# Optimization experiments

Hardware: AMD Instinct MI355X
Metric: run time of the kernel (lower is better)

Reference implementation:

```python
import jax, jax.numpy as jnp
import numpy as np

# static config
B, H, W, C = 32, 56, 56, 128
WH, WW = 7, 7
SH, SW = 3, 3
NH = 4            # num heads
HD = C // NH      # head dim = 32
N = WH * WW       # 49 tokens per window
NWIN = (H // WH) * (W // WW)  # 64 windows
MLP_H = int(C * 4.0)
EPS = 1e-6
SCALE = HD ** -0.5


def _rel_pos_index():
    ch, cw = np.arange(WH), np.arange(WW)
    co = np.stack(np.meshgrid(ch, cw, indexing='ij')).reshape(2, -1)
    rc = (co[:, :, None] - co[:, None, :]).transpose(1, 2, 0)
    rc[:, :, 0] += WH - 1
    rc[:, :, 1] += WW - 1
    rc[:, :, 0] *= 2 * WW - 1
    return rc.sum(-1)  # [N, N] int


def _attn_mask():
    img = np.zeros((1, H, W, 1), np.float32)
    cnt = 0
    for hs in (slice(0, -WH), slice(-WH, -SH), slice(-SH, None)):
        for ws in (slice(0, -WW), slice(-WW, -SW), slice(-SW, None)):
            img[:, hs, ws, :] = cnt
            cnt += 1
    mw = img.reshape(1, H // WH, WH, W // WW, WW, 1)
    mw = mw.transpose(0, 1, 3, 2, 4, 5).reshape(-1, N)  # [nW, N]
    am = mw[:, None, :] - mw[:, :, None]
    return np.where(am != 0, -100.0, 0.0).astype(np.float32)  # [nW, N, N]

REL_IDX = jnp.asarray(_rel_pos_index())
ATTN_MASK = jnp.asarray(_attn_mask())


def _ln(x, g, b):
    mu = jnp.mean(x, -1, keepdims=True)
    var = jnp.mean(jnp.square(x - mu), -1, keepdims=True)
    return (x - mu) * jax.lax.rsqrt(var + EPS) * g + b


def _part(x):  # [B,H,W,C] -> [B*nW, N, C]
    x = x.reshape(B, H // WH, WH, W // WW, WW, C)
    return x.transpose(0, 1, 3, 2, 4, 5).reshape(-1, N, C)


def _rev(w):  # [B*nW, N, C] -> [B,H,W,C]
    x = w.reshape(B, H // WH, W // WW, WH, WW, C)
    return x.transpose(0, 1, 3, 2, 4, 5).reshape(B, H, W, C)


def setup_inputs() -> dict:
    key = jax.random.key(0)
    ks = jax.random.split(key, 16)
    s = lambda k, sh, sc=0.02: jax.random.normal(k, sh, jnp.float32) * sc
    return {
        'x': jax.random.normal(ks[0], (B, H * W, C), jnp.float32),
        'qkv_w': s(ks[1], (C, 3 * C)),
        'qkv_b': jnp.zeros((3 * C,), jnp.float32),
        'proj_w': s(ks[2], (C, C)),
        'proj_b': jnp.zeros((C,), jnp.float32),
        'proj_ln_g': jnp.ones((C,), jnp.float32),
        'proj_ln_b': jnp.zeros((C,), jnp.float32),
        'rpb_table': s(ks[3], ((2 * WH - 1) * (2 * WW - 1), NH)),
        'norm1_g': jnp.ones((C,), jnp.float32),
        'norm1_b': jnp.zeros((C,), jnp.float32),
        'norm2_g': jnp.ones((C,), jnp.float32),
        'norm2_b': jnp.zeros((C,), jnp.float32),
        'mlp_w1': s(ks[4], (C, MLP_H)),
        'mlp_b1': jnp.zeros((MLP_H,), jnp.float32),
        'mlp_w2': s(ks[5], (MLP_H, C)),
        'mlp_b2': jnp.zeros((C,), jnp.float32),
    }


def reference(x, qkv_w, qkv_b, proj_w, proj_b, proj_ln_g, proj_ln_b, rpb_table,
              norm1_g, norm1_b, norm2_g, norm2_b, mlp_w1, mlp_b1, mlp_w2, mlp_b2):
    shortcut = x
    h = _ln(x, norm1_g, norm1_b).reshape(B, H, W, C)
    h = jnp.roll(h, shift=(-SH, -SW), axis=(1, 2))        # cyclic shift
    w = _part(h)                                          # [B*nW, N, C]

    qkv = w @ qkv_w + qkv_b                               # [B*nW, N, 3C]
    qkv = qkv.reshape(-1, N, 3, NH, HD).transpose(2, 0, 3, 1, 4)
    q, k, v = qkv[0] * SCALE, qkv[1], qkv[2]              # [B*nW, NH, N, HD]
    attn = jnp.einsum('bhnd,bhmd->bhnm', q, k)            # [B*nW, NH, N, N]

    bias = rpb_table[REL_IDX.reshape(-1)].reshape(N, N, NH).transpose(2, 0, 1)
    attn = attn + bias[None]

    # masked path (shifted windows): NOTE source applies softmax TWICE — faithful
    attn = attn.reshape(-1, NWIN, NH, N, N) + ATTN_MASK[None, :, None]
    attn = jax.nn.softmax(attn, axis=-1)
    attn = attn.reshape(-1, NH, N, N)
    attn = jax.nn.softmax(attn, axis=-1)

    o = jnp.einsum('bhnm,bhmd->bhnd', attn, v)
    o = o.transpose(0, 2, 1, 3).reshape(-1, N, C)
    # projection: Dense -> LayerNorm -> GELU (as in source WindowAttention)
    o = jax.nn.gelu(_ln(o @ proj_w + proj_b, proj_ln_g, proj_ln_b), approximate=False)

    h = _rev(o)
    h = jnp.roll(h, shift=(SH, SW), axis=(1, 2)).reshape(B, H * W, C)
    x = shortcut + h

    m = _ln(x, norm2_g, norm2_b)
    m = jax.nn.gelu(m @ mlp_w1 + mlp_b1, approximate=False) @ mlp_w2 + mlp_b2
    return x + m
```

## Files before the change

### kernel.cpp

```cpp
#include <hip/hip_runtime.h>
#include <cstdint>
#include <cstddef>

typedef __attribute__((ext_vector_type(8))) short bf16x8;
typedef __attribute__((ext_vector_type(4))) float f32x4;
typedef unsigned char uchar;

namespace {
constexpr float kScale = 0.17677669529663689f;
constexpr float kEps = 1e-6f;
constexpr float kInvC = 1.0f / 128.0f;

__device__ __forceinline__ float gelu_fast(float v) {
  float t1 = fmaf(0.044715f * v, v, 1.0f);
  float x = v * t1 * -1.5957691216057308f;
  float e = __expf(x);
  return v * __builtin_amdgcn_rcpf(1.0f + e);
}
__device__ __forceinline__ float gelu_sig(float v) {
  float e = __expf(-1.702f * v);
  return v * __builtin_amdgcn_rcpf(1.0f + e);
}
__device__ __forceinline__ ushort f2bf(float f) {
  uint32_t u = __builtin_bit_cast(uint32_t, f);
  u += 0x7FFFu + ((u >> 16) & 1u);
  return (ushort)(u >> 16);
}
__device__ __forceinline__ float bf2f(ushort u) {
  return __builtin_bit_cast(float, (uint32_t)u << 16);
}
__device__ __forceinline__ void gl16(const void* g, void* l) {
  __builtin_amdgcn_global_load_lds(
      (const __attribute__((address_space(1))) void*)g,
      (__attribute__((address_space(3))) void*)l, 16, 0, 0);
}
__device__ __forceinline__ int map_row(int t) {
  int win = t / 49, nn = t - win * 49;
  int bb = win >> 6, wi = win & 63;
  int whi = wi >> 3, wwi = wi & 7;
  int r7 = nn / 7, c7 = nn - r7 * 7;
  int hs = whi * 7 + r7 + 3; if (hs >= 56) hs -= 56;
  int wsd = wwi * 7 + c7 + 3; if (wsd >= 56) wsd -= 56;
  return bb * 3136 + hs * 56 + wsd;
}
}

__global__ __launch_bounds__(256) void k_prep(
    const float* __restrict__ qkv_w, const float* __restrict__ w1,
    const float* __restrict__ w2, const float* __restrict__ pw,
    ushort* __restrict__ qkvT, ushort* __restrict__ w1T,
    uchar* __restrict__ w2T8, ushort* __restrict__ projT) {
  int i = blockIdx.x * 256 + threadIdx.x;
  if (i < 49152) {
    int n = i >> 7, k = i & 127;
    qkvT[i] = f2bf(qkv_w[k * 384 + n]);
  } else if (i < 114688) {
    int j = i - 49152;
    int n = j >> 7, k = j & 127;
    w1T[j] = f2bf(w1[k * 512 + n]);
  } else if (i < 147456) {
    int j = i - 114688;
    int n = j >> 8, k2 = (j & 255) << 1;
    int u = __builtin_amdgcn_cvt_pk_fp8_f32(w2[(size_t)k2 * 128 + n],
                                            w2[(size_t)(k2 + 1) * 128 + n], 0,
                                            false);
    w2T8[n * 512 + k2] = (uchar)u;
    w2T8[n * 512 + k2 + 1] = (uchar)(u >> 8);
  } else if (i < 163840) {
    int j = i - 147456;
    int n = j >> 7, k = j & 127;
    projT[j] = f2bf(pw[k * 128 + n]);
  }
}

__global__ __launch_bounds__(256) void k_prep2(
    const float* __restrict__ rpb, float* __restrict__ TB) {
  int e = blockIdx.x * 256 + threadIdx.x;
  int i = e & 63, j = (e >> 6) & 63, h = (e >> 12) & 3, type = e >> 14;
  float v = 0.f;
  if (i < 49 && j < 49) {
    int ri = i / 7, ci = i - ri * 7, rj = j / 7, cj = j - rj * 7;
    int ridx = (ri - rj + 6) * 13 + (ci - cj + 6);
    float bias = rpb[ridx * 4 + h];
    int th = type >> 1, tw = type & 1;
    int labi = (th ? ((ri < 4) ? 1 : 2) : 0) * 3 + (tw ? ((ci < 4) ? 1 : 2) : 0);
    int labj = (th ? ((rj < 4) ? 1 : 2) : 0) * 3 + (tw ? ((cj < 4) ? 1 : 2) : 0);
    v = bias + ((labi != labj) ? -100.f : 0.f);
  }
  TB[e] = v;
}

__global__ __launch_bounds__(256) void k_ln1_part(
    const float* __restrict__ x, const float* __restrict__ g,
    const float* __restrict__ b, ushort* __restrict__ wp) {
  int lane = threadIdx.x & 63, wv = threadIdx.x >> 6;
  int half = lane >> 5, l32 = lane & 31;
  int tok = blockIdx.x * 8 + wv * 2 + half;
  size_t src = (size_t)map_row(tok) * 128;
  float4 v = *(const float4*)(x + src + l32 * 4);
  float s = v.x + v.y + v.z + v.w;
  float sq = v.x * v.x + v.y * v.y + v.z * v.z + v.w * v.w;
#pragma unroll
  for (int off = 1; off < 32; off <<= 1) {
    s += __shfl_xor(s, off);
    sq += __shfl_xor(sq, off);
  }
  float mu = s * kInvC;
  float var = sq * kInvC - mu * mu;
  float rs = rsqrtf(var + kEps);
  float4 gg = *(const float4*)(g + l32 * 4);
  float4 bv = *(const float4*)(b + l32 * 4);
  float o0 = (v.x - mu) * rs * gg.x + bv.x;
  float o1 = (v.y - mu) * rs * gg.y + bv.y;
  float o2 = (v.z - mu) * rs * gg.z + bv.z;
  float o3 = (v.w - mu) * rs * gg.w + bv.w;
  uint2 p;
  p.x = (uint)f2bf(o0) | ((uint)f2bf(o1) << 16);
  p.y = (uint)f2bf(o2) | ((uint)f2bf(o3) << 16);
  ((uint2*)wp)[(size_t)tok * 32 + l32] = p;
}

template <int K, int LDC, int EPI>
__global__ __launch_bounds__(256) void k_gemm2(
    const ushort* __restrict__ A, const ushort* __restrict__ BT,
    const float* __restrict__ bias, ushort* __restrict__ C) {
  __shared__ ushort sbuf[12288];
  int tid = threadIdx.x;
  int nBase = blockIdx.x << 7;
  int mBase = blockIdx.y << 6;
  int lane = tid & 63, wid = tid >> 6;
  int li = lane & 15, g = lane >> 4;
  int wr = (wid >> 1) << 5, wc = (wid & 1) << 6;
  int swz = (li & 7) << 3;
  f32x4 acc[2][4] = {};
  for (int ks = 0; ks < K; ks += 64) {
#pragma unroll
    for (int l = 0; l < 2; ++l) {
      int c = l * 256 + tid;
      int row = c >> 3;
      int k8 = ((c & 7) ^ (row & 7)) << 3;
      gl16(A + (size_t)(mBase + row) * K + ks + k8,
           sbuf + (l * 256 + wid * 64) * 8);
    }
#pragma unroll
    for (int l = 0; l < 4; ++l) {
      int c = l * 256 + tid;
      int row = c >> 3;
      int k8 = ((c & 7) ^ (row & 7)) << 3;
      gl16(BT + (size_t)(nBase + row) * K + ks + k8,
           sbuf + 4096 + (l * 256 + wid * 64) * 8);
    }
    __syncthreads();
#pragma unroll
    for (int ksub = 0; ksub < 64; ksub += 32) {
      int kloc = ksub + g * 8;
      bf16x8 af[2], bfr[4];
#pragma unroll
      for (int m = 0; m < 2; ++m)
        af[m] = *(const bf16x8*)(sbuf + (wr + m * 16 + li) * 64 + (kloc ^ swz));
#pragma unroll
      for (int n = 0; n < 4; ++n)
        bfr[n] = *(const bf16x8*)(sbuf + 4096 + (wc + n * 16 + li) * 64 +
                                  (kloc ^ swz));
#pragma unroll
      for (int m = 0; m < 2; ++m)
#pragma unroll
        for (int n = 0; n < 4; ++n)
          acc[m][n] = __builtin_amdgcn_mfma_f32_16x16x32_bf16(
              af[m], bfr[n], acc[m][n], 0, 0, 0);
    }
    __syncthreads();
  }
#pragma unroll
  for (int n = 0; n < 4; ++n) {
    float bv = bias[nBase + wc + n * 16 + li];
    int col = wc + n * 16 + li;
#pragma unroll
    for (int m = 0; m < 2; ++m) {
      int rb = wr + m * 16 + (g << 2);
#pragma unroll
      for (int r = 0; r < 4; ++r) {
        float v = acc[m][n][r] + bv;
        if (EPI == 1) v = gelu_fast(v);
        sbuf[(rb + r) * 136 + col] = f2bf(v);
      }
    }
  }
  __syncthreads();
#pragma unroll
  for (int it = 0; it < 4; ++it) {
    int ch = tid + it * 256;
    int row = ch >> 4, c8 = (ch & 15) << 3;
    *(bf16x8*)(C + (size_t)(mBase + row) * LDC + nBase + c8) =
        *(const bf16x8*)(sbuf + row * 136 + c8);
  }
}

__global__ __launch_bounds__(256) void k_mlp1(
    const ushort* __restrict__ A, const ushort* __restrict__ BT,
    const float* __restrict__ bias, uchar* __restrict__ C8) {
  __shared__ ushort sbuf[12288];
  int tid = threadIdx.x;
  int nBase = blockIdx.x << 7;
  int mBase = blockIdx.y << 6;
  int lane = tid & 63, wid = tid >> 6;
  int li = lane & 15, g = lane >> 4;
  int wr = (wid >> 1) << 5, wc = (wid & 1) << 6;
  int swz = (li & 7) << 3;
  f32x4 acc[2][4] = {};
  for (int ks = 0; ks < 128; ks += 64) {
#pragma unroll
    for (int l = 0; l < 2; ++l) {
      int c = l * 256 + tid;
      int row = c >> 3;
      int k8 = ((c & 7) ^ (row & 7)) << 3;
      gl16(A + (size_t)(mBase + row) * 128 + ks + k8,
           sbuf + (l * 256 + wid * 64) * 8);
    }
#pragma unroll
    for (int l = 0; l < 4; ++l) {
      int c = l * 256 + tid;
      int row = c >> 3;
      int k8 = ((c & 7) ^ (row & 7)) << 3;
      gl16(BT + (size_t)(nBase + row) * 128 + ks + k8,
           sbuf + 4096 + (l * 256 + wid * 64) * 8);
    }
    __syncthreads();
#pragma unroll
    for (int ksub = 0; ksub < 64; ksub += 32) {
      int kloc = ksub + g * 8;
      bf16x8 af[2], bfr[4];
#pragma unroll
      for (int m = 0; m < 2; ++m)
        af[m] = *(const bf16x8*)(sbuf + (wr + m * 16 + li) * 64 + (kloc ^ swz));
#pragma unroll
      for (int n = 0; n < 4; ++n)
        bfr[n] = *(const bf16x8*)(sbuf + 4096 + (wc + n * 16 + li) * 64 +
                                  (kloc ^ swz));
#pragma unroll
      for (int m = 0; m < 2; ++m)
#pragma unroll
        for (int n = 0; n < 4; ++n)
          acc[m][n] = __builtin_amdgcn_mfma_f32_16x16x32_bf16(
              af[m], bfr[n], acc[m][n], 0, 0, 0);
    }
    __syncthreads();
  }
  uchar* Cs8 = (uchar*)sbuf;
#pragma unroll
  for (int n = 0; n < 4; ++n) {
    float bv = bias[nBase + wc + n * 16 + li];
    int col = wc + n * 16 + li;
#pragma unroll
    for (int m = 0; m < 2; ++m) {
      int rb = wr + m * 16 + (g << 2);
      float v0 = gelu_sig(acc[m][n][0] + bv);
      float v1 = gelu_sig(acc[m][n][1] + bv);
      float v2 = gelu_sig(acc[m][n][2] + bv);
      float v3 = gelu_sig(acc[m][n][3] + bv);
      int u01 = __builtin_amdgcn_cvt_pk_fp8_f32(v0, v1, 0, false);
      int u23 = __builtin_amdgcn_cvt_pk_fp8_f32(v2, v3, 0, false);
      Cs8[(rb + 0) * 144 + col] = (uchar)u01;
      Cs8[(rb + 1) * 144 + col] = (uchar)(u01 >> 8);
      Cs8[(rb + 2) * 144 + col] = (uchar)u23;
      Cs8[(rb + 3) * 144 + col] = (uchar)(u23 >> 8);
    }
  }
  __syncthreads();
#pragma unroll
  for (int it = 0; it < 2; ++it) {
    int ch = tid + it * 256;
    int row = ch >> 3, c16 = (ch & 7) << 4;
    *(bf16x8*)(C8 + (size_t)(mBase + row) * 512 + nBase + c16) =
        *(const bf16x8*)(Cs8 + row * 144 + c16);
  }
}

__global__ __launch_bounds__(256) void k_mlp2(
    const uchar* __restrict__ A8, const uchar* __restrict__ BT8,
    const float* __restrict__ bias, const ushort* __restrict__ resw,
    float* __restrict__ out) {
  __shared__ uchar sbuf[32768];
  __shared__ int mapr[64];
  int tid = threadIdx.x;
  int mBase = blockIdx.x << 6;
  if (tid < 64) mapr[tid] = map_row(mBase + tid);
  int lane = tid & 63, wid = tid >> 6;
  int li = lane & 15, g = lane >> 4;
  int wr = (wid >> 1) << 5, wc = (wid & 1) << 6;
  f32x4 acc[2][4] = {};
  for (int kb = 0; kb < 512; kb += 128) {
#pragma unroll
    for (int l = 0; l < 2; ++l) {
      int c = l * 256 + tid;
      int row = c >> 3;
      int ch = (c & 7) ^ (row & 7);
      gl16(A8 + (size_t)(mBase + row) * 512 + kb + (ch << 4),
           sbuf + (l * 256 + wid * 64) * 16);
    }
#pragma unroll
    for (int l = 0; l < 4; ++l) {
      int c = l * 256 + tid;
      int row = c >> 3;
      int ch = (c & 7) ^ (row & 7);
      gl16(BT8 + (size_t)row * 512 + kb + (ch << 4),
           sbuf + 8192 + (l * 256 + wid * 64) * 16);
    }
    __syncthreads();
#pragma unroll
    for (int ks = 0; ks < 4; ++ks) {
      int off = ks * 32 + g * 8;
      long long af[2], bfr[4];
#pragma unroll
      for (int m = 0; m < 2; ++m) {
        int r = wr + m * 16 + li;
        af[m] = *(const long long*)(sbuf + r * 128 + (off ^ ((r & 7) << 4)));
      }
#pragma unroll
      for (int n = 0; n < 4; ++n) {
        int rb = wc + n * 16 + li;
        bfr[n] = *(const long long*)(sbuf + 8192 + rb * 128 +
                                     (off ^ ((rb & 7) << 4)));
      }
#pragma unroll
      for (int m = 0; m < 2; ++m)
#pragma unroll
        for (int n = 0; n < 4; ++n)
          acc[m][n] = __builtin_amdgcn_mfma_f32_16x16x32_fp8_fp8(
              af[m], bfr[n], acc[m][n], 0, 0, 0);
    }
    __syncthreads();
  }
  float (*outs)[128] = (float(*)[128])sbuf;
#pragma unroll
  for (int n = 0; n < 4; ++n) {
    int cg = wc + n * 16 + li;
    float bv = bias[cg];
#pragma unroll
    for (int m = 0; m < 2; ++m) {
      int rb = wr + m * 16 + (g << 2);
#pragma unroll
      for (int r = 0; r < 4; ++r) {
        float rv = bf2f(resw[(size_t)(mBase + rb + r) * 128 + cg]);
        outs[rb + r][cg] = rv + acc[m][n][r] + bv;
      }
    }
  }
  __syncthreads();
#pragma unroll
  for (int it = 0; it < 8; ++it) {
    int ch = tid + it * 256;
    int row = ch >> 5, c4 = (ch & 31) << 2;
    *(float4*)(out + (size_t)mapr[row] * 128 + c4) =
        *(const float4*)&outs[row][c4];
  }
}

__global__ __launch_bounds__(256) void k_pgemm(
    const ushort* __restrict__ A, const ushort* __restrict__ BT,
    const float* __restrict__ pb, const float* __restrict__ lg,
    const float* __restrict__ lb, const float* __restrict__ x,
    const float* __restrict__ g2, const float* __restrict__ b2n,
    ushort* __restrict__ resw, ushort* __restrict__ wp) {
  __shared__ ushort sbuf[16384];
  __shared__ float red[4][64][2];
  __shared__ int mapr[64];
  int tid = threadIdx.x;
  int mBase = blockIdx.x << 6;
  if (tid < 64) mapr[tid] = map_row(mBase + tid);
  int lane = tid & 63, wid = tid >> 6;
  int li = lane & 15, g = lane >> 4;
  int wr = (wid >> 1) << 5, wc = (wid & 1) << 6;
  int swz = (li & 7) << 3;
  f32x4 acc[2][4] = {};
  for (int ks = 0; ks < 128; ks += 64) {
#pragma unroll
    for (int l = 0; l < 2; ++l) {
      int c = l * 256 + tid;
      int row = c >> 3;
      int k8 = ((c & 7) ^ (row & 7)) << 3;
      gl16(A + (size_t)(mBase + row) * 128 + ks + k8,
           sbuf + (l * 256 + wid * 64) * 8);
    }
#pragma unroll
    for (int l = 0; l < 4; ++l) {
      int c = l * 256 + tid;
      int row = c >> 3;
      int k8 = ((c & 7) ^ (row & 7)) << 3;
      gl16(BT + (size_t)row * 128 + ks + k8,
           sbuf + 4096 + (l * 256 + wid * 64) * 8);
    }
    __syncthreads();
#pragma unroll
    for (int ksub = 0; ksub < 64; ksub += 32) {
      int kloc = ksub + g * 8;
      bf16x8 af[2], bfr[4];
#pragma unroll
      for (int m = 0; m < 2; ++m)
        af[m] = *(const bf16x8*)(sbuf + (wr + m * 16 + li) * 64 + (kloc ^ swz));
#pragma unroll
      for (int n = 0; n < 4; ++n)
        bfr[n] = *(const bf16x8*)(sbuf + 4096 + (wc + n * 16 + li) * 64 +
                                  (kloc ^ swz));
#pragma unroll
      for (int m = 0; m < 2; ++m)
#pragma unroll
        for (int n = 0; n < 4; ++n)
          acc[m][n] = __builtin_amdgcn_mfma_f32_16x16x32_bf16(
              af[m], bfr[n], acc[m][n], 0, 0, 0);
    }
    __syncthreads();
  }
  float pbv[4], lgv[4], lbv[4], g2v[4], b2v[4];
#pragma unroll
  for (int n = 0; n < 4; ++n) {
    int cg = wc + n * 16 + li;
    pbv[n] = pb[cg]; lgv[n] = lg[cg]; lbv[n] = lb[cg];
    g2v[n] = g2[cg]; b2v[n] = b2n[cg];
  }
  float ps[2][4], psq[2][4];
#pragma unroll
  for (int m = 0; m < 2; ++m)
#pragma unroll
    for (int r = 0; r < 4; ++r) {
      float s = 0.f, q = 0.f;
#pragma unroll
      for (int n = 0; n < 4; ++n) {
        float v = acc[m][n][r] + pbv[n];
        s += v; q += v * v;
      }
#pragma unroll
      for (int off = 1; off < 16; off <<= 1) {
        s += __shfl_xor(s, off);
        q += __shfl_xor(q, off);
      }
      ps[m][r] = s; psq[m][r] = q;
    }
  if (li == 0) {
#pragma unroll
    for (int m = 0; m < 2; ++m)
#pragma unroll
      for (int r = 0; r < 4; ++r) {
        int rl = wr + m * 16 + (g << 2) + r;
        red[wid][rl][0] = ps[m][r];
        red[wid][rl][1] = psq[m][r];
      }
  }
  __syncthreads();
  float mu1[2][4], rs1[2][4];
#pragma unroll
  for (int m = 0; m < 2; ++m)
#pragma unroll
    for (int r = 0; r < 4; ++r) {
      int rl = wr + m * 16 + (g << 2) + r;
      float s = ps[m][r] + red[wid ^ 1][rl][0];
      float q = psq[m][r] + red[wid ^ 1][rl][1];
      mu1[m][r] = s * kInvC;
      rs1[m][r] = rsqrtf(q * kInvC - mu1[m][r] * mu1[m][r] + kEps);
    }
  __syncthreads();
#pragma unroll
  for (int m = 0; m < 2; ++m)
#pragma unroll
    for (int r = 0; r < 4; ++r) {
      int rowl = wr + m * 16 + (g << 2) + r;
      size_t xb = (size_t)mapr[rowl] * 128 + wc + li;
#pragma unroll
      for (int n = 0; n < 4; ++n) {
        float y = (acc[m][n][r] + pbv[n] - mu1[m][r]) * rs1[m][r] * lgv[n] +
                  lbv[n];
        acc[m][n][r] = gelu_fast(y) + x[xb + n * 16];
      }
    }
#pragma unroll
  for (int m = 0; m < 2; ++m)
#pragma unroll
    for (int r = 0; r < 4; ++r) {
      float s = 0.f, q = 0.f;
#pragma unroll
      for (int n = 0; n < 4; ++n) {
        float v = acc[m][n][r];
        s += v; q += v * v;
      }
#pragma unroll
      for (int off = 1; off < 16; off <<= 1) {
        s += __shfl_xor(s, off);
        q += __shfl_xor(q, off);
      }
      ps[m][r] = s; psq[m][r] = q;
    }
  if (li == 0) {
#pragma unroll
    for (int m = 0; m < 2; ++m)
#pragma unroll
      for (int r = 0; r < 4; ++r) {
        int rl = wr + m * 16 + (g << 2) + r;
        red[wid][rl][0] = ps[m][r];
        red[wid][rl][1] = psq[m][r];
      }
  }
  __syncthreads();
  ushort (*Cr)[128] = (ushort(*)[128])sbuf;
  ushort (*Cw)[128] = (ushort(*)[128])(sbuf + 8192);
#pragma unroll
  for (int m = 0; m < 2; ++m)
#pragma unroll
    for (int r = 0; r < 4; ++r) {
      int rl = wr + m * 16 + (g << 2) + r;
      float s = ps[m][r] + red[wid ^ 1][rl][0];
      float q = psq[m][r] + red[wid ^ 1][rl][1];
      float mu = s * kInvC;
      float rs = rsqrtf(q * kInvC - mu * mu + kEps);
#pragma unroll
      for (int n = 0; n < 4; ++n) {
        int col = wc + n * 16 + li;
        float rv = acc[m][n][r];
        Cr[rl][col] = f2bf(rv);
        Cw[rl][col] = f2bf((rv - mu) * rs * g2v[n] + b2v[n]);
      }
    }
  __syncthreads();
#pragma unroll
  for (int it = 0; it < 4; ++it) {
    int ch = tid + it * 256;
    int row = ch >> 4, c8 = (ch & 15) << 3;
    *(bf16x8*)(resw + (size_t)(mBase + row) * 128 + c8) =
        *(const bf16x8*)&Cr[row][c8];
    *(bf16x8*)(wp + (size_t)(mBase + row) * 128 + c8) =
        *(const bf16x8*)&Cw[row][c8];
  }
}

__global__ __launch_bounds__(256) void k_attn(
    const ushort* __restrict__ qkv, const float* __restrict__ TB,
    ushort* __restrict__ ob) {
  __shared__ ushort Pl[4][64][68];
  __shared__ ushort Vt[4][32][68];
  int tid = threadIdx.x;
  int lane = tid & 63, h = tid >> 6;
  int li = lane & 15, g = lane >> 4;
  int win = blockIdx.x;
  int wi = win & 63;
  int type = (((wi >> 3) == 7) ? 2 : 0) | (((wi & 7) == 7) ? 1 : 0);

  const ushort* qbase = qkv + (size_t)win * 49 * 384 + h * 32 + g * 8;
  bf16x8 kf[4], qf[4];
#pragma unroll
  for (int m = 0; m < 4; ++m) {
    kf[m] = *(const bf16x8*)(qbase + (size_t)(m * 16 + li) * 384 + 128);
    qf[m] = *(const bf16x8*)(qbase + (size_t)(m * 16 + li) * 384);
  }
  f32x4 zero = {0.f, 0.f, 0.f, 0.f};
  f32x4 st[4][4];
#pragma unroll
  for (int m = 0; m < 4; ++m)
#pragma unroll
    for (int n = 0; n < 4; ++n)
      st[m][n] = __builtin_amdgcn_mfma_f32_16x16x32_bf16(kf[m], qf[n], zero, 0, 0, 0);

  if (lane < 49) {
#pragma unroll
    for (int dc = 0; dc < 4; ++dc) {
      bf16x8 vv = *(const bf16x8*)(qkv + ((size_t)win * 49 + lane) * 384 + 256 +
                                   h * 32 + dc * 8);
#pragma unroll
      for (int t = 0; t < 8; ++t) Vt[h][dc * 8 + t][lane] = (ushort)vv[t];
    }
  } else {
#pragma unroll
    for (int d = 0; d < 32; ++d) Vt[h][d][lane] = 0;
  }

  const float* tb = TB + ((size_t)(type * 4 + h) << 12);
#pragma unroll
  for (int n = 0; n < 4; ++n) {
    int icol = n * 16 + li;
    float sv[3][4];
#pragma unroll
    for (int m = 0; m < 3; ++m)
#pragma unroll
      for (int r = 0; r < 4; ++r)
        sv[m][r] = st[m][n][r] * kScale + tb[(m * 16 + g * 4 + r) * 64 + icol];
    float sv3 = (g == 0) ? (st[3][n][0] * kScale + tb[48 * 64 + icol]) : -1e30f;
    float e[3][4], e3 = __expf(sv3);
    float sum = e3;
#pragma unroll
    for (int m = 0; m < 3; ++m)
#pragma unroll
      for (int r = 0; r < 4; ++r) { e[m][r] = __expf(sv[m][r]); sum += e[m][r]; }
    sum += __shfl_xor(sum, 16);
    sum += __shfl_xor(sum, 32);
    float inv = 1.f / sum;
    float e2[3][4];
    float e23 = (g == 0) ? __expf(e3 * inv) : 0.f;
    float sum2 = e23;
#pragma unroll
    for (int m = 0; m < 3; ++m)
#pragma unroll
      for (int r = 0; r < 4; ++r) { e2[m][r] = __expf(e[m][r] * inv); sum2 += e2[m][r]; }
    sum2 += __shfl_xor(sum2, 16);
    sum2 += __shfl_xor(sum2, 32);
    float inv2 = 1.f / sum2;
#pragma unroll
    for (int m = 0; m < 3; ++m) {
      uint u0 = (uint)f2bf(e2[m][0] * inv2) | ((uint)f2bf(e2[m][1] * inv2) << 16);
      uint u1 = (uint)f2bf(e2[m][2] * inv2) | ((uint)f2bf(e2[m][3] * inv2) << 16);
      *(uint*)&Pl[h][icol][m * 16 + g * 4]     = u0;
      *(uint*)&Pl[h][icol][m * 16 + g * 4 + 2] = u1;
    }
    uint u3 = (g == 0) ? (uint)f2bf(e23 * inv2) : 0u;
    *(uint*)&Pl[h][icol][48 + g * 4]     = u3;
    *(uint*)&Pl[h][icol][48 + g * 4 + 2] = 0u;
  }
  __syncthreads();

  f32x4 oacc[4][2] = {};
#pragma unroll
  for (int ks = 0; ks < 2; ++ks) {
    int kloc = ks * 32 + g * 8;
    bf16x8 bf0 = *(const bf16x8*)&Vt[h][li][kloc];
    bf16x8 bf1 = *(const bf16x8*)&Vt[h][16 + li][kloc];
#pragma unroll
    for (int mi = 0; mi < 4; ++mi) {
      bf16x8 af = *(const bf16x8*)&Pl[h][mi * 16 + li][kloc];
      oacc[mi][0] = __builtin_amdgcn_mfma_f32_16x16x32_bf16(af, bf0, oacc[mi][0], 0, 0, 0);
      oacc[mi][1] = __builtin_amdgcn_mfma_f32_16x16x32_bf16(af, bf1, oacc[mi][1], 0, 0, 0);
    }
  }
  ushort* OlH = &Pl[h][0][0];
#pragma unroll
  for (int mi = 0; mi < 4; ++mi)
#pragma unroll
    for (int r = 0; r < 4; ++r) {
      int i = mi * 16 + g * 4 + r;
      if (mi < 3 || (g == 0 && r == 0)) {
        OlH[i * 40 + li]      = f2bf(oacc[mi][0][r]);
        OlH[i * 40 + 16 + li] = f2bf(oacc[mi][1][r]);
      }
    }
  __syncthreads();
  ushort* obase = ob + (size_t)win * 49 * 128;
#pragma unroll
  for (int it = 0; it < 4; ++it) {
    int chunk = tid + it * 256;
    if (chunk < 784) {
      int row = chunk >> 4, c8 = (chunk & 15) << 3;
      int h2 = c8 >> 5, d8 = c8 & 31;
      bf16x8 v = *(const bf16x8*)(&Pl[h2][0][0] + row * 40 + d8);
      *(bf16x8*)(obase + (size_t)row * 128 + c8) = v;
    }
  }
}

extern "C" void kernel_launch(void* const* d_in, const int* in_sizes, int n_in,
                              void* d_out, int out_size, void* d_ws,
                              size_t ws_size, hipStream_t stream) {
  (void)in_sizes; (void)n_in; (void)out_size; (void)ws_size;
  const float* x      = (const float*)d_in[0];
  const float* qkv_w  = (const float*)d_in[1];
  const float* qkv_b  = (const float*)d_in[2];
  const float* proj_w = (const float*)d_in[3];
  const float* proj_b = (const float*)d_in[4];
  const float* plg    = (const float*)d_in[5];
  const float* plb    = (const float*)d_in[6];
  const float* rpb    = (const float*)d_in[7];
  const float* n1g    = (const float*)d_in[8];
  const float* n1b    = (const float*)d_in[9];
  const float* n2g    = (const float*)d_in[10];
  const float* n2b    = (const float*)d_in[11];
  const float* w1     = (const float*)d_in[12];
  const float* b1     = (const float*)d_in[13];
  const float* w2     = (const float*)d_in[14];
  const float* b2     = (const float*)d_in[15];
  float* out = (float*)d_out;

  ushort* wp   = (ushort*)d_ws;
  ushort* qkvb = wp + (size_t)100352 * 128;
  ushort* obb  = qkvb + (size_t)100352 * 384;
  uchar*  hb8  = (uchar*)(obb + (size_t)100352 * 128);
  ushort* qkvT = (ushort*)(hb8 + (size_t)100352 * 512);
  ushort* w1T  = qkvT + 384 * 128;
  uchar*  w2T8 = (uchar*)(w1T + 512 * 128);
  ushort* pT   = (ushort*)(w2T8 + 128 * 512);
  float*  TB   = (float*)(pT + 128 * 128);
  ushort* resw = qkvb;

  k_prep<<<640, 256, 0, stream>>>(qkv_w, w1, w2, proj_w, qkvT, w1T, w2T8, pT);
  k_prep2<<<256, 256, 0, stream>>>(rpb, TB);
  k_ln1_part<<<12544, 256, 0, stream>>>(x, n1g, n1b, wp);
  k_gemm2<128, 384, 0><<<dim3(3, 1568), 256, 0, stream>>>(wp, qkvT, qkv_b, qkvb);
  k_attn<<<2048, 256, 0, stream>>>(qkvb, TB, obb);
  k_pgemm<<<1568, 256, 0, stream>>>(obb, pT, proj_b, plg, plb, x, n2g, n2b,
                                    resw, wp);
  k_mlp1<<<dim3(4, 1568), 256, 0, stream>>>(wp, w1T, b1, hb8);
  k_mlp2<<<1568, 256, 0, stream>>>(hb8, w2T8, b2, resw, out);
}
```

Measured before the change: 168.6 us.

## Fuse LayerNorm1 and window partition into the QKV GEMM prologue

Removes the separate LN1+partition kernel and its bf16 intermediate buffer. The QKV GEMM now gathers each row of x through map_row, computes LayerNorm statistics with four threads per row, normalizes, and writes bf16 tiles straight into swizzled shared memory. The write and re-read of the normalized activations and one launch go away. In exchange, each of the three N-blocks repeats the LayerNorm and reads the fp32 x rows again, which triples x traffic into the GEMM.

```diff
diff --git a/kernel.cpp b/kernel.cpp
--- a/kernel.cpp
+++ b/kernel.cpp
@@ -90,65 +90,66 @@
   TB[e] = v;
 }
 
-__global__ __launch_bounds__(256) void k_ln1_part(
-    const float* __restrict__ x, const float* __restrict__ g,
-    const float* __restrict__ b, ushort* __restrict__ wp) {
-  int lane = threadIdx.x & 63, wv = threadIdx.x >> 6;
-  int half = lane >> 5, l32 = lane & 31;
-  int tok = blockIdx.x * 8 + wv * 2 + half;
-  size_t src = (size_t)map_row(tok) * 128;
-  float4 v = *(const float4*)(x + src + l32 * 4);
-  float s = v.x + v.y + v.z + v.w;
-  float sq = v.x * v.x + v.y * v.y + v.z * v.z + v.w * v.w;
-#pragma unroll
-  for (int off = 1; off < 32; off <<= 1) {
-    s += __shfl_xor(s, off);
-    sq += __shfl_xor(sq, off);
-  }
-  float mu = s * kInvC;
-  float var = sq * kInvC - mu * mu;
-  float rs = rsqrtf(var + kEps);
-  float4 gg = *(const float4*)(g + l32 * 4);
-  float4 bv = *(const float4*)(b + l32 * 4);
-  float o0 = (v.x - mu) * rs * gg.x + bv.x;
-  float o1 = (v.y - mu) * rs * gg.y + bv.y;
-  float o2 = (v.z - mu) * rs * gg.z + bv.z;
-  float o3 = (v.w - mu) * rs * gg.w + bv.w;
-  uint2 p;
-  p.x = (uint)f2bf(o0) | ((uint)f2bf(o1) << 16);
-  p.y = (uint)f2bf(o2) | ((uint)f2bf(o3) << 16);
-  ((uint2*)wp)[(size_t)tok * 32 + l32] = p;
-}
-
-template <int K, int LDC, int EPI>
-__global__ __launch_bounds__(256) void k_gemm2(
-    const ushort* __restrict__ A, const ushort* __restrict__ BT,
+__global__ __launch_bounds__(256) void k_qkvf(
+    const float* __restrict__ x, const float* __restrict__ g1,
+    const float* __restrict__ b1, const ushort* __restrict__ BT,
     const float* __restrict__ bias, ushort* __restrict__ C) {
   __shared__ ushort sbuf[12288];
+  __shared__ int mapr[64];
   int tid = threadIdx.x;
   int nBase = blockIdx.x << 7;
   int mBase = blockIdx.y << 6;
+  if (tid < 64) mapr[tid] = map_row(mBase + tid);
   int lane = tid & 63, wid = tid >> 6;
   int li = lane & 15, g = lane >> 4;
   int wr = (wid >> 1) << 5, wc = (wid & 1) << 6;
   int swz = (li & 7) << 3;
+  int r = tid >> 2, q = tid & 3;
+  __syncthreads();
+  const float* xr = x + (size_t)mapr[r] * 128;
+  float s = 0.f, sq = 0.f;
+#pragma unroll
+  for (int j = 0; j < 8; ++j) {
+    float4 v = *(const float4*)(xr + q * 32 + j * 4);
+    s += v.x + v.y + v.z + v.w;
+    sq += v.x * v.x + v.y * v.y + v.z * v.z + v.w * v.w;
+  }
+  s += __shfl_xor(s, 1); s += __shfl_xor(s, 2);
+  sq += __shfl_xor(sq, 1); sq += __shfl_xor(sq, 2);
+  float mu = s * kInvC;
+  float rs = rsqrtf(sq * kInvC - mu * mu + kEps);
   f32x4 acc[2][4] = {};
-  for (int ks = 0; ks < K; ks += 64) {
-#pragma unroll
-    for (int l = 0; l < 2; ++l) {
-      int c = l * 256 + tid;
-      int row = c >> 3;
-      int k8 = ((c & 7) ^ (row & 7)) << 3;
-      gl16(A + (size_t)(mBase + row) * K + ks + k8,
-           sbuf + (l * 256 + wid * 64) * 8);
-    }
+#pragma unroll
+  for (int h = 0; h < 2; ++h) {
+    int ks = h << 6;
 #pragma unroll
     for (int l = 0; l < 4; ++l) {
       int c = l * 256 + tid;
       int row = c >> 3;
       int k8 = ((c & 7) ^ (row & 7)) << 3;
-      gl16(BT + (size_t)(nBase + row) * K + ks + k8,
+      gl16(BT + (size_t)(nBase + row) * 128 + ks + k8,
            sbuf + 4096 + (l * 256 + wid * 64) * 8);
+    }
+#pragma unroll
+    for (int c2 = 0; c2 < 2; ++c2) {
+      int cc = ks + q * 16 + c2 * 8;
+      float4 v0 = *(const float4*)(xr + cc);
+      float4 v1 = *(const float4*)(xr + cc + 4);
+      float4 gg0 = *(const float4*)(g1 + cc);
+      float4 gg1 = *(const float4*)(g1 + cc + 4);
+      float4 bb0 = *(const float4*)(b1 + cc);
+      float4 bb1 = *(const float4*)(b1 + cc + 4);
+      bf16x8 pk;
+      pk[0] = (short)f2bf((v0.x - mu) * rs * gg0.x + bb0.x);
+      pk[1] = (short)f2bf((v0.y - mu) * rs * gg0.y + bb0.y);
+      pk[2] = (short)f2bf((v0.z - mu) * rs * gg0.z + bb0.z);
+      pk[3] = (short)f2bf((v0.w - mu) * rs * gg0.w + bb0.w);
+      pk[4] = (short)f2bf((v1.x - mu) * rs * gg1.x + bb1.x);
+      pk[5] = (short)f2bf((v1.y - mu) * rs * gg1.y + bb1.y);
+      pk[6] = (short)f2bf((v1.z - mu) * rs * gg1.z + bb1.z);
+      pk[7] = (short)f2bf((v1.w - mu) * rs * gg1.w + bb1.w);
+      int ch = (cc - ks) >> 3;
+      *(bf16x8*)(sbuf + r * 64 + ((ch ^ (r & 7)) << 3)) = pk;
     }
     __syncthreads();
 #pragma unroll
@@ -179,11 +180,8 @@
     for (int m = 0; m < 2; ++m) {
       int rb = wr + m * 16 + (g << 2);
 #pragma unroll
-      for (int r = 0; r < 4; ++r) {
-        float v = acc[m][n][r] + bv;
-        if (EPI == 1) v = gelu_fast(v);
-        sbuf[(rb + r) * 136 + col] = f2bf(v);
-      }
+      for (int rr = 0; rr < 4; ++rr)
+        sbuf[(rb + rr) * 136 + col] = f2bf(acc[m][n][rr] + bv);
     }
   }
   __syncthreads();
@@ -191,7 +189,7 @@
   for (int it = 0; it < 4; ++it) {
     int ch = tid + it * 256;
     int row = ch >> 4, c8 = (ch & 15) << 3;
-    *(bf16x8*)(C + (size_t)(mBase + row) * LDC + nBase + c8) =
+    *(bf16x8*)(C + (size_t)(mBase + row) * 384 + nBase + c8) =
         *(const bf16x8*)(sbuf + row * 136 + c8);
   }
 }
@@ -687,8 +685,7 @@
 
   k_prep<<<640, 256, 0, stream>>>(qkv_w, w1, w2, proj_w, qkvT, w1T, w2T8, pT);
   k_prep2<<<256, 256, 0, stream>>>(rpb, TB);
-  k_ln1_part<<<12544, 256, 0, stream>>>(x, n1g, n1b, wp);
-  k_gemm2<128, 384, 0><<<dim3(3, 1568), 256, 0, stream>>>(wp, qkvT, qkv_b, qkvb);
+  k_qkvf<<<dim3(3, 1568), 256, 0, stream>>>(x, n1g, n1b, qkvT, qkv_b, qkvb);
   k_attn<<<2048, 256, 0, stream>>>(qkvb, TB, obb);
   k_pgemm<<<1568, 256, 0, stream>>>(obb, pT, proj_b, plg, plb, x, n2g, n2b,
                                     resw, wp);
```

Result: slower. 187.7 us (+11.3%).
